# Performance work log

Hardware: AMD Instinct MI355X
Metric: run time of the kernel (lower is better)

## Reference

```python
import jax, jax.numpy as jnp
import numpy as np

B, D, Q, E, H, V = 32, 1024, 64, 384, 384, 50000
PAD = 0
EPS = 1e-12


def setup_inputs() -> dict:
    key = jax.random.key(0)
    ks = jax.random.split(key, 13)
    documents = jax.random.randint(ks[0], (B, D), 1, V)
    doc_lens = jax.random.randint(ks[1], (B,), D // 2, D + 1)
    doc_valid = jnp.arange(D)[None, :] < doc_lens[:, None]
    documents = jnp.where(doc_valid, documents, PAD)
    doc_masks = doc_valid.astype(jnp.float32)[:, :, None]
    querys = jax.random.randint(ks[2], (B, Q), 1, V)
    query_lens = jax.random.randint(ks[3], (B,), Q // 2, Q + 1)
    q_valid = jnp.arange(Q)[None, :] < query_lens[:, None]
    querys = jnp.where(q_valid, querys, PAD)
    query_masks = q_valid.astype(jnp.float32)[:, :, None]
    answers = documents[:, :1]  # guaranteed present in each doc
    emb = jax.random.uniform(ks[4], (V + 1, E), jnp.float32, -0.05, 0.05)
    emb = emb.at[PAD].set(0.0)
    gw = lambda k, s: jax.random.normal(k, s, jnp.float32) * 0.05
    w_ih_f = gw(ks[5], (3 * H, E)); w_hh_f = gw(ks[6], (3 * H, H))
    b_ih_f = gw(ks[7], (3 * H,)); b_hh_f = gw(ks[8], (3 * H,))
    w_ih_b = gw(ks[9], (3 * H, E)); w_hh_b = gw(ks[10], (3 * H, H))
    b_ih_b = gw(ks[11], (3 * H,)); b_hh_b = gw(ks[12], (3 * H,))
    return dict(documents=documents, doc_lens=doc_lens, doc_masks=doc_masks,
                querys=querys, query_lens=query_lens, query_masks=query_masks,
                answers=answers, emb=emb,
                w_ih_f=w_ih_f, w_hh_f=w_hh_f, b_ih_f=b_ih_f, b_hh_f=b_hh_f,
                w_ih_b=w_ih_b, w_hh_b=w_hh_b, b_ih_b=b_ih_b, b_hh_b=b_hh_b)


def _gru_dir(x, w_ih, w_hh, b_ih, b_hh):
    # x: [B,T,E] -> outputs [B,T,H]; torch GRU cell math
    Bn = x.shape[0]
    Hn = w_hh.shape[1]
    xp = jnp.einsum('bte,ge->btg', x, w_ih) + b_ih  # precompute input projections [B,T,3H]

    def step(h, g):
        gh = h @ w_hh.T + b_hh
        i_r, i_z, i_n = jnp.split(g, 3, axis=-1)
        h_r, h_z, h_n = jnp.split(gh, 3, axis=-1)
        r = jax.nn.sigmoid(i_r + h_r)
        z = jax.nn.sigmoid(i_z + h_z)
        n = jnp.tanh(i_n + r * h_n)
        hn = (1.0 - z) * n + z * h
        return hn, hn

    h0 = jnp.zeros((Bn, Hn), x.dtype)
    _, out = jax.lax.scan(step, h0, jnp.swapaxes(xp, 0, 1))
    return jnp.swapaxes(out, 0, 1)


def _rev_within_len(x, lens):
    # reverse each sequence only over its valid prefix (emulates packed bwd GRU)
    T = x.shape[1]
    t = jnp.arange(T)
    idx = jnp.where(t[None, :] < lens[:, None], lens[:, None] - 1 - t[None, :], t[None, :])
    return jnp.take_along_axis(x, idx[:, :, None], axis=1)


def _bigru(x, lens, valid, pf, pb):
    out_f = _gru_dir(x, *pf)
    out_b = _rev_within_len(_gru_dir(_rev_within_len(x, lens), *pb), lens)
    out = jnp.concatenate([out_f, out_b], axis=-1)
    return out * valid[:, :, None]  # unpack pads with zeros


def _softmax_mask(x, mask, axis):
    shift = jnp.max(x, axis=axis, keepdims=True)
    e = jnp.exp(x - shift) * mask
    return e / (jnp.sum(e, axis=axis, keepdims=True) + EPS)


def reference(documents, doc_lens, doc_masks, querys, query_lens, query_masks, answers,
              emb, w_ih_f, w_hh_f, b_ih_f, b_hh_f, w_ih_b, w_hh_b, b_ih_b, b_hh_b):
    doc_valid = doc_masks[..., 0]
    q_valid = query_masks[..., 0]
    doc_h = _bigru(emb[documents], doc_lens, doc_valid,
                   (w_ih_f, w_hh_f, b_ih_f, b_hh_f), (w_ih_b, w_hh_b, b_ih_b, b_hh_b))
    q_h = _bigru(emb[querys], query_lens, q_valid,
                 (w_ih_f, w_hh_f, b_ih_f, b_hh_f), (w_ih_b, w_hh_b, b_ih_b, b_hh_b))
    scores = jnp.einsum('bdh,bqh->bdq', doc_h, q_h)          # IndiATT_output
    pair_mask = jnp.einsum('bdo,bqo->bdq', doc_masks, query_masks)
    alpha = _softmax_mask(scores, pair_mask, axis=1)
    beta = _softmax_mask(scores, pair_mask, axis=2)
    beta_aver = jnp.sum(beta, axis=1) / doc_lens[:, None].astype(scores.dtype)  # [B,Q]
    s = jnp.einsum('bdq,bq->bd', alpha, beta_aver)            # AoA_output squeezed
    probs = jnp.sum(s * (documents == answers).astype(s.dtype), axis=1)

    def pick(doc, sv, vv):
        sc = jnp.zeros(V + 1, s.dtype).at[doc].add(sv * vv)   # segment-sum by word id
        cnt = jnp.zeros(V + 1, s.dtype).at[doc].add(vv)
        return jnp.argmax(jnp.where(cnt > 0, sc, -jnp.inf))

    pred_answers = jax.vmap(pick)(documents, s, doc_valid)
    return probs, pred_answers
```

## Files before the change

### kernel.cpp

```cpp
#include <hip/hip_runtime.h>
#include <hip/hip_bf16.h>
#include <stdint.h>

#define EPSV 1e-12f
#define NB 32
#define DD 1024
#define QQ 64
#define EE 384
#define HH 384
#define NW 12

typedef __attribute__((ext_vector_type(4))) float f32x4;
typedef __attribute__((ext_vector_type(8))) __bf16 bf16x8;
typedef __attribute__((ext_vector_type(4))) unsigned short u16x4;
typedef __attribute__((ext_vector_type(4))) int i32x4;
typedef unsigned short u16;

static __device__ __forceinline__ u16 f2bf(float f) {
  union { float f; uint32_t u; } v; v.f = f;
  uint32_t u = v.u;
  return (u16)((u + 0x7fffu + ((u >> 16) & 1u)) >> 16);
}

static __device__ __forceinline__ f32x4 MFMA(bf16x8 a, bf16x8 b, f32x4 c) {
  return __builtin_amdgcn_mfma_f32_16x16x32_bf16(a, b, c, 0, 0, 0);
}

static __device__ __forceinline__ void st_short_sc(u16* p, u16 v) {
  asm volatile("global_store_short %0, %1, off sc1" :: "v"(p), "v"((uint32_t)v) : "memory");
}
static __device__ __forceinline__ void ld_b128_sc(const u16* p, i32x4& d) {
  asm volatile("global_load_dwordx4 %0, %1, off sc1" : "=v"(d) : "v"(p) : "memory");
}

__global__ __launch_bounds__(256) void k_emb(const int* __restrict__ doc, const int* __restrict__ qry,
                                             const float* __restrict__ emb, u16* __restrict__ embx) {
  int i = blockIdx.x * 256 + threadIdx.x;
  int row = i / 96, e4 = i - row * 96;
  int tok = (row < NB * DD) ? doc[row] : qry[row - NB * DD];
  float4 v = ((const float4*)(emb + (size_t)tok * EE))[e4];
  u16x4 o; o.x = f2bf(v.x); o.y = f2bf(v.y); o.z = f2bf(v.z); o.w = f2bf(v.w);
  *(u16x4*)(embx + (size_t)row * EE + e4 * 4) = o;
}

__global__ __launch_bounds__(256) void k_rec(
    const u16* __restrict__ embx,
    const int* __restrict__ doc_lens, const int* __restrict__ q_lens,
    const float* __restrict__ w_ih_f, const float* __restrict__ w_hh_f,
    const float* __restrict__ b_ih_f, const float* __restrict__ b_hh_f,
    const float* __restrict__ w_ih_b, const float* __restrict__ w_hh_b,
    const float* __restrict__ b_ih_b, const float* __restrict__ b_hh_b,
    u16* __restrict__ doc_h, u16* __restrict__ q_h,
    u16* __restrict__ h_bc, unsigned* __restrict__ cnts) {
  __shared__ u16 wfrag[73728];
  __shared__ int lensh[32];

  const int grp = blockIdx.x / NW;
  const int wg = blockIdx.x - grp * NW;
  const int corpus = grp >> 1, dir = grp & 1;
  const int T = corpus ? QQ : DD;
  const int* lens = corpus ? q_lens : doc_lens;
  const float* w_ih = dir ? w_ih_b : w_ih_f;
  const float* w_hh = dir ? w_hh_b : w_hh_f;
  const float* b_ih = dir ? b_ih_b : b_ih_f;
  const float* b_hh = dir ? b_hh_b : b_hh_f;
  u16* out = corpus ? q_h : doc_h;
  const u16* ex_base = embx + (corpus ? (size_t)NB * DD * EE : 0);
  u16* hb = h_bc + (size_t)grp * (2 * NB * HH);
  unsigned* cnt = cnts + (size_t)grp * (1056 * 16);
  const int tid = threadIdx.x;

  if (tid < 32) lensh[tid] = lens[tid];
  for (int idx = tid; idx < 73728; idx += 256) {
    int nt = idx / 12288;
    int rem = idx - nt * 12288;
    int ks = rem >> 9;
    int le = rem & 511;
    int lane_ = le >> 3, i = le & 7;
    int g = nt >> 1, js_ = nt & 1;
    int colw = lane_ & 15, khiw = lane_ >> 4;
    int k = ks * 32 + khiw * 8 + i;
    int rowg = g * 384 + wg * 32 + js_ * 16 + colw;
    float v = (k < 384) ? w_ih[rowg * 384 + k] : w_hh[rowg * 384 + (k - 384)];
    wfrag[idx] = f2bf(v);
  }
  for (int idx = tid; idx < 1024; idx += 256) {
    int b = idx >> 5, jl_ = idx & 31;
    st_short_sc(hb + b * HH + wg * 32 + jl_, (u16)0);
  }
  asm volatile("s_waitcnt vmcnt(0)" ::: "memory");
  __syncthreads();
  if (tid == 0) {
    __hip_atomic_fetch_add(cnt, 1u, __ATOMIC_RELAXED, __HIP_MEMORY_SCOPE_AGENT);
    while (__hip_atomic_load(cnt, __ATOMIC_RELAXED, __HIP_MEMORY_SCOPE_AGENT) < (unsigned)NW)
      __builtin_amdgcn_s_sleep(1);
  }
  __syncthreads();

  const int lane = tid & 63, wv = tid >> 6;
  const int mt = wv >> 1, js = wv & 1;
  const int col = lane & 15, khi = lane >> 4;
  const int jg = wg * 32 + js * 16 + col;
  const float bias_r = b_ih[jg] + b_hh[jg];
  const float bias_z = b_ih[384 + jg] + b_hh[384 + jg];
  const float bias_in = b_ih[768 + jg];
  const float bias_hn = b_hh[768 + jg];
  const int b_x = mt * 16 + col;
  const int len_x = lensh[b_x];
  const int bh0 = mt * 16 + khi * 4;
  int len_h[4];
#pragma unroll
  for (int r = 0; r < 4; ++r) len_h[r] = lensh[bh0 + r];
  const u16* exrow = ex_base + (size_t)b_x * T * EE + khi * 8;
  u16* outp = out + (size_t)dir * HH + jg;
  f32x4 hprev{0.f, 0.f, 0.f, 0.f};

  auto trow_of = [&](int s) -> int { return dir ? ((s < len_x) ? (len_x - 1 - s) : s) : s; };
  auto load_ax = [&](bf16x8* ax, int s) {
    const u16* axp = exrow + (size_t)trow_of(s) * EE;
#pragma unroll
    for (int ks = 0; ks < 12; ++ks) ax[ks] = *(const bf16x8*)(axp + ks * 32);
  };

  bf16x8 axA[12], axB[12];
  load_ax(axA, 0);

  auto step = [&](int s, bf16x8* axc, bf16x8* axn) {
    const int p = s & 1;
    const u16* rbuf = hb + p * (NB * HH);
    u16* wbuf = hb + (p ^ 1) * (NB * HH);
    if (s + 1 < T) load_ax(axn, s + 1);
    i32x4 areg[12];
    const u16* ahp = rbuf + b_x * HH + khi * 8;
#pragma unroll
    for (int ks = 0; ks < 12; ++ks) ld_b128_sc(ahp + ks * 32, areg[ks]);
    f32x4 acc_r{0.f, 0.f, 0.f, 0.f};
    f32x4 acc_z = acc_r, acc_nx = acc_r, acc_nh = acc_r;
#pragma unroll
    for (int ks = 0; ks < 12; ++ks) {
      bf16x8 br = *(const bf16x8*)&wfrag[((js) * 24 + ks) * 512 + lane * 8];
      bf16x8 bz = *(const bf16x8*)&wfrag[((2 + js) * 24 + ks) * 512 + lane * 8];
      bf16x8 bn = *(const bf16x8*)&wfrag[((4 + js) * 24 + ks) * 512 + lane * 8];
      acc_r = MFMA(axc[ks], br, acc_r);
      acc_z = MFMA(axc[ks], bz, acc_z);
      acc_nx = MFMA(axc[ks], bn, acc_nx);
    }
    asm volatile("s_waitcnt vmcnt(0)" ::: "memory");
    __builtin_amdgcn_sched_barrier(0);
#pragma unroll
    for (int ks = 0; ks < 12; ++ks) {
      bf16x8 af = __builtin_bit_cast(bf16x8, areg[ks]);
      bf16x8 br = *(const bf16x8*)&wfrag[((js) * 24 + 12 + ks) * 512 + lane * 8];
      bf16x8 bz = *(const bf16x8*)&wfrag[((2 + js) * 24 + 12 + ks) * 512 + lane * 8];
      bf16x8 bn = *(const bf16x8*)&wfrag[((4 + js) * 24 + 12 + ks) * 512 + lane * 8];
      acc_r = MFMA(af, br, acc_r);
      acc_z = MFMA(af, bz, acc_z);
      acc_nh = MFMA(af, bn, acc_nh);
    }
#pragma unroll
    for (int r = 0; r < 4; ++r) {
      const int b = bh0 + r;
      float rg = 1.f / (1.f + __expf(-(acc_r[r] + bias_r)));
      float zg = 1.f / (1.f + __expf(-(acc_z[r] + bias_z)));
      float ng = tanhf(acc_nx[r] + bias_in + rg * (acc_nh[r] + bias_hn));
      float hn = (1.f - zg) * ng + zg * hprev[r];
      hprev[r] = hn;
      u16 hq = f2bf(hn);
      st_short_sc(wbuf + b * HH + jg, hq);
      const int len = len_h[r];
      const int tro = dir ? ((s < len) ? (len - 1 - s) : s) : s;
      outp[((size_t)b * T + tro) * (2 * HH)] = hq;
    }
    asm volatile("s_waitcnt vmcnt(0)" ::: "memory");
    __syncthreads();
    if (tid == 0) {
      unsigned* c = cnt + (size_t)(s + 1) * 16;
      __hip_atomic_fetch_add(c, 1u, __ATOMIC_RELAXED, __HIP_MEMORY_SCOPE_AGENT);
      while (__hip_atomic_load(c, __ATOMIC_RELAXED, __HIP_MEMORY_SCOPE_AGENT) < (unsigned)NW)
        __builtin_amdgcn_s_sleep(1);
    }
    __syncthreads();
  };

  for (int s = 0; s < T; s += 2) {
    step(s, axA, axB);
    step(s + 1, axB, axA);
  }
}

__global__ __launch_bounds__(256) void k_scores(
    const u16* __restrict__ doc_h, const u16* __restrict__ q_h,
    const int* __restrict__ doc_lens, const int* __restrict__ q_lens,
    float* __restrict__ SM, float* __restrict__ rowmax, float* __restrict__ rowsum) {
  const int b = blockIdx.x >> 4, dblk = blockIdx.x & 15;
  const int tid = threadIdx.x, lane = tid & 63, wv = tid >> 6;
  const int col = lane & 15, khi = lane >> 4;
  const int dlen = doc_lens[b], qlen = q_lens[b];
  const u16* dp = doc_h + ((size_t)(b * DD + dblk * 64 + wv * 16 + col)) * (2 * HH) + khi * 8;
  const u16* qp = q_h + (size_t)b * QQ * (2 * HH);
  f32x4 acc[4];
#pragma unroll
  for (int nt = 0; nt < 4; ++nt) acc[nt] = f32x4{0.f, 0.f, 0.f, 0.f};
  for (int ks = 0; ks < 24; ++ks) {
    bf16x8 av = *(const bf16x8*)(dp + ks * 32);
#pragma unroll
    for (int nt = 0; nt < 4; ++nt) {
      bf16x8 bv = *(const bf16x8*)(qp + (size_t)(nt * 16 + col) * (2 * HH) + ks * 32 + khi * 8);
      acc[nt] = MFMA(av, bv, acc[nt]);
    }
  }
  const int d0 = dblk * 64 + wv * 16 + khi * 4;
  float* smb = SM + (size_t)b * DD * QQ;
#pragma unroll
  for (int r = 0; r < 4; ++r) {
    const int d = d0 + r;
    const bool dv = d < dlen;
    float v[4];
#pragma unroll
    for (int nt = 0; nt < 4; ++nt) {
      const int q = nt * 16 + col;
      v[nt] = (dv && q < qlen) ? acc[nt][r] : 0.f;
      smb[(size_t)d * QQ + q] = v[nt];
    }
    float mx = fmaxf(fmaxf(v[0], v[1]), fmaxf(v[2], v[3]));
#pragma unroll
    for (int off = 1; off < 16; off <<= 1) mx = fmaxf(mx, __shfl_xor(mx, off, 64));
    float sm = 0.f;
#pragma unroll
    for (int nt = 0; nt < 4; ++nt) {
      const int q = nt * 16 + col;
      if (dv && q < qlen) sm += __expf(v[nt] - mx);
    }
#pragma unroll
    for (int off = 1; off < 16; off <<= 1) sm += __shfl_xor(sm, off, 64);
    if (col == 0) { rowmax[b * DD + d] = mx; rowsum[b * DD + d] = sm; }
  }
}

__global__ __launch_bounds__(256) void k_cols(
    const float* __restrict__ SM, const float* __restrict__ rowmax, const float* __restrict__ rowsum,
    const int* __restrict__ doc_lens, const int* __restrict__ q_lens,
    float* __restrict__ colmax, float* __restrict__ colsum, float* __restrict__ bav) {
  const int b = blockIdx.x, tid = threadIdx.x;
  const int q = tid & 63, dg = tid >> 6;
  __shared__ float red[4][64];
  __shared__ float cmx[64];
  const float* smb = SM + (size_t)b * DD * QQ;
  float cm = -3.0e38f;
  for (int d = dg; d < DD; d += 4) cm = fmaxf(cm, smb[(size_t)d * QQ + q]);
  red[dg][q] = cm;
  __syncthreads();
  if (tid < 64) cmx[tid] = fmaxf(fmaxf(red[0][tid], red[1][tid]), fmaxf(red[2][tid], red[3][tid]));
  __syncthreads();
  const int dlen = doc_lens[b];
  const bool qv = q < q_lens[b];
  const float cmq = cmx[q];
  float cs = 0.f, ba = 0.f;
  for (int d = dg; d < DD; d += 4) {
    if (qv && d < dlen) {
      float v = smb[(size_t)d * QQ + q];
      cs += __expf(v - cmq);
      ba += __expf(v - rowmax[b * DD + d]) / (rowsum[b * DD + d] + EPSV);
    }
  }
  __syncthreads();
  red[dg][q] = cs;
  __syncthreads();
  float cst = 0.f;
  if (tid < 64) cst = red[0][tid] + red[1][tid] + red[2][tid] + red[3][tid];
  __syncthreads();
  red[dg][q] = ba;
  __syncthreads();
  if (tid < 64) {
    float bat = red[0][tid] + red[1][tid] + red[2][tid] + red[3][tid];
    colmax[b * QQ + tid] = cmx[tid];
    colsum[b * QQ + tid] = cst;
    bav[b * QQ + tid] = bat / (float)dlen;
  }
}

__global__ __launch_bounds__(256) void k_s(
    const float* __restrict__ SM, const float* __restrict__ colmax, const float* __restrict__ colsum,
    const float* __restrict__ bav, const int* __restrict__ doc_lens, const int* __restrict__ q_lens,
    const int* __restrict__ documents, const int* __restrict__ answers,
    float* __restrict__ sc, float* __restrict__ cnt_tok, float* __restrict__ dout) {
  const int b = blockIdx.x >> 2, dblk = blockIdx.x & 3;
  const int tid = threadIdx.x;
  __shared__ float cm[64], cs[64], bv[64];
  __shared__ int qm[64];
  if (tid < 64) {
    cm[tid] = colmax[b * QQ + tid];
    cs[tid] = colsum[b * QQ + tid];
    bv[tid] = bav[b * QQ + tid];
    qm[tid] = (tid < q_lens[b]) ? 1 : 0;
  }
  __syncthreads();
  const int d = dblk * 256 + tid;
  const bool dv = d < doc_lens[b];
  const float* smr = SM + ((size_t)b * DD + d) * QQ;
  float sd = 0.f;
#pragma unroll
  for (int q = 0; q < 64; ++q) {
    float e = (dv && qm[q]) ? __expf(smr[q] - cm[q]) : 0.f;
    sd += e / (cs[q] + EPSV) * bv[q];
  }
  const int tok = documents[b * DD + d];
  if (tok == answers[b]) atomicAdd(&dout[b], sd);
  if (dv) {
    atomicAdd(&sc[(size_t)b * 50001 + tok], sd);
    atomicAdd(&cnt_tok[(size_t)b * 50001 + tok], 1.0f);
  }
}

__global__ __launch_bounds__(256) void k_pred(
    const float* __restrict__ sc, const float* __restrict__ cnt_tok, float* __restrict__ dout) {
  const int b = blockIdx.x, tid = threadIdx.x;
  __shared__ float bvs[256];
  __shared__ int bis[256];
  float bvv = -3.0e38f;
  int bii = 0x7fffffff;
  for (int i = tid; i < 50001; i += 256) {
    if (cnt_tok[(size_t)b * 50001 + i] > 0.f) {
      float v = sc[(size_t)b * 50001 + i];
      if (v > bvv) { bvv = v; bii = i; }
    }
  }
  bvs[tid] = bvv;
  bis[tid] = bii;
  __syncthreads();
  for (int st = 128; st > 0; st >>= 1) {
    if (tid < st) {
      float v2 = bvs[tid + st];
      int i2 = bis[tid + st];
      if (v2 > bvs[tid] || (v2 == bvs[tid] && i2 < bis[tid])) { bvs[tid] = v2; bis[tid] = i2; }
    }
    __syncthreads();
  }
  if (tid == 0) dout[32 + b] = (float)bis[0];
}

extern "C" void kernel_launch(void* const* d_in, const int* in_sizes, int n_in,
                              void* d_out, int out_size, void* d_ws, size_t ws_size,
                              hipStream_t stream) {
  const int* documents = (const int*)d_in[0];
  const int* doc_lens = (const int*)d_in[1];
  const int* querys = (const int*)d_in[3];
  const int* query_lens = (const int*)d_in[4];
  const int* answers = (const int*)d_in[6];
  const float* emb = (const float*)d_in[7];
  const float* w_ih_f = (const float*)d_in[8];
  const float* w_hh_f = (const float*)d_in[9];
  const float* b_ih_f = (const float*)d_in[10];
  const float* b_hh_f = (const float*)d_in[11];
  const float* w_ih_b = (const float*)d_in[12];
  const float* w_hh_b = (const float*)d_in[13];
  const float* b_ih_b = (const float*)d_in[14];
  const float* b_hh_b = (const float*)d_in[15];
  float* dout = (float*)d_out;
  char* ws = (char*)d_ws;

  size_t o = 0;
  auto alloc = [&](size_t bytes) { size_t r = o; o += (bytes + 255) & ~(size_t)255; return r; };
  size_t o_embx = alloc((size_t)34816 * 384 * 2);
  size_t o_doch = alloc((size_t)NB * DD * 768 * 2);
  size_t o_qh   = alloc((size_t)NB * QQ * 768 * 2);
  size_t o_hbc  = alloc((size_t)4 * 2 * NB * HH * 2);
  size_t o_cnt  = alloc((size_t)4 * 1056 * 16 * 4);
  size_t o_SM   = alloc((size_t)NB * DD * QQ * 4);
  size_t o_rmax = alloc((size_t)NB * DD * 4);
  size_t o_rsum = alloc((size_t)NB * DD * 4);
  size_t o_cmax = alloc((size_t)NB * QQ * 4);
  size_t o_csum = alloc((size_t)NB * QQ * 4);
  size_t o_bav  = alloc((size_t)NB * QQ * 4);
  size_t o_sc   = alloc((size_t)NB * 50001 * 4);
  size_t o_ctk  = alloc((size_t)NB * 50001 * 4);
  (void)ws_size; (void)in_sizes; (void)n_in; (void)out_size;

  hipMemsetAsync(ws + o_cnt, 0, (size_t)4 * 1056 * 16 * 4, stream);
  hipMemsetAsync(ws + o_sc, 0, (o_ctk - o_sc) + (size_t)NB * 50001 * 4, stream);
  hipMemsetAsync(d_out, 0, 64 * sizeof(float), stream);

  k_emb<<<13056, 256, 0, stream>>>(documents, querys, emb, (u16*)(ws + o_embx));
  k_rec<<<48, 256, 0, stream>>>((u16*)(ws + o_embx), doc_lens, query_lens,
                                w_ih_f, w_hh_f, b_ih_f, b_hh_f,
                                w_ih_b, w_hh_b, b_ih_b, b_hh_b,
                                (u16*)(ws + o_doch), (u16*)(ws + o_qh),
                                (u16*)(ws + o_hbc), (unsigned*)(ws + o_cnt));
  k_scores<<<512, 256, 0, stream>>>((u16*)(ws + o_doch), (u16*)(ws + o_qh), doc_lens, query_lens,
                                    (float*)(ws + o_SM), (float*)(ws + o_rmax), (float*)(ws + o_rsum));
  k_cols<<<32, 256, 0, stream>>>((float*)(ws + o_SM), (float*)(ws + o_rmax), (float*)(ws + o_rsum),
                                 doc_lens, query_lens,
                                 (float*)(ws + o_cmax), (float*)(ws + o_csum), (float*)(ws + o_bav));
  k_s<<<128, 256, 0, stream>>>((float*)(ws + o_SM), (float*)(ws + o_cmax), (float*)(ws + o_csum),
                               (float*)(ws + o_bav), doc_lens, query_lens, documents, answers,
                               (float*)(ws + o_sc), (float*)(ws + o_ctk), dout);
  k_pred<<<32, 256, 0, stream>>>((float*)(ws + o_sc), (float*)(ws + o_ctk), dout);
}
```

Before: 6.000 ms.

## Hoist GRU input projections into chunked parallel kernel, shrink recurrent grid

The input projection (x·W_ih) is moved out of the sequential GRU loop into a separate parallel MFMA kernel that writes fp32 gate pre-activations in chunks of 256 timesteps. The recurrent kernel now does only the h·W_hh product with 4 workgroups per direction instead of 12, so fewer blocks take part in each per-step global barrier. The r-gate weights stay in registers and the z and n gate weights sit in LDS. Hidden state is carried across four launches through a global buffer. This cuts per-step MFMA work and sync fan-in, but each workgroup handles more columns per step, and the change adds launches and xp memory traffic.

```diff
diff --git a/kernel.cpp b/kernel.cpp
--- a/kernel.cpp
+++ b/kernel.cpp
@@ -8,7 +8,8 @@
 #define QQ 64
 #define EE 384
 #define HH 384
-#define NW 12
+#define NWR 4
+#define CH 256
 
 typedef __attribute__((ext_vector_type(4))) float f32x4;
 typedef __attribute__((ext_vector_type(8))) __bf16 bf16x8;
@@ -24,6 +25,15 @@
 
 static __device__ __forceinline__ f32x4 MFMA(bf16x8 a, bf16x8 b, f32x4 c) {
   return __builtin_amdgcn_mfma_f32_16x16x32_bf16(a, b, c, 0, 0, 0);
+}
+
+static __device__ __forceinline__ bf16x8 ldw8(const float* p) {
+  float4 a = *(const float4*)p;
+  float4 b = *(const float4*)(p + 4);
+  union { u16 e[8]; bf16x8 v; } u;
+  u.e[0] = f2bf(a.x); u.e[1] = f2bf(a.y); u.e[2] = f2bf(a.z); u.e[3] = f2bf(a.w);
+  u.e[4] = f2bf(b.x); u.e[5] = f2bf(b.y); u.e[6] = f2bf(b.z); u.e[7] = f2bf(b.w);
+  return u.v;
 }
 
 static __device__ __forceinline__ void st_short_sc(u16* p, u16 v) {
@@ -43,149 +53,223 @@
   *(u16x4*)(embx + (size_t)row * EE + e4 * 4) = o;
 }
 
-__global__ __launch_bounds__(256) void k_rec(
-    const u16* __restrict__ embx,
+__global__ __launch_bounds__(512, 2) void k_xp(
+    const u16* __restrict__ embx, const int* __restrict__ doc_lens, const int* __restrict__ q_lens,
+    const float* __restrict__ w_ih_f, const float* __restrict__ b_ih_f, const float* __restrict__ b_hh_f,
+    const float* __restrict__ w_ih_b, const float* __restrict__ b_ih_b, const float* __restrict__ b_hh_b,
+    float* __restrict__ xpd, float* __restrict__ xpq, int cbase) {
+  __shared__ int lensh[32];
+  const int gx = blockIdx.x;
+  int corpus, d2, jblk, tch;
+  if (gx < 48) { corpus = 0; d2 = gx / 24; int rem = gx % 24; jblk = rem / 4; tch = rem % 4; }
+  else { corpus = 1; int g2 = gx - 48; d2 = g2 / 6; jblk = g2 % 6; tch = 0; }
+  const int T = corpus ? QQ : DD;
+  const int* lens = corpus ? q_lens : doc_lens;
+  const float* w_ih = d2 ? w_ih_b : w_ih_f;
+  const float* b_ih = d2 ? b_ih_b : b_ih_f;
+  const float* b_hh = d2 ? b_hh_b : b_hh_f;
+  const u16* exb = embx + (corpus ? (size_t)NB * DD * EE : 0);
+  float* xpg = corpus ? (xpq + (size_t)d2 * QQ * 36864) : (xpd + (size_t)d2 * CH * 36864);
+  const int tid = threadIdx.x;
+  if (tid < 32) lensh[tid] = lens[tid];
+  __syncthreads();
+  const int lane = tid & 63, wv = tid >> 6;
+  const int wslot = wv >> 1, mt = wv & 1;
+  const int col = lane & 15, khi = lane >> 4;
+  const int jg = jblk * 64 + wslot * 16 + col;
+  const float br = b_ih[jg] + b_hh[jg];
+  const float bz = b_ih[384 + jg] + b_hh[384 + jg];
+  const float bn = b_ih[768 + jg];
+  bf16x8 Wr[12], Wz[12], Wn[12];
+#pragma unroll
+  for (int ks = 0; ks < 12; ++ks) {
+    Wr[ks] = ldw8(w_ih + (size_t)jg * 384 + ks * 32 + khi * 8);
+    Wz[ks] = ldw8(w_ih + (size_t)(384 + jg) * 384 + ks * 32 + khi * 8);
+    Wn[ks] = ldw8(w_ih + (size_t)(768 + jg) * 384 + ks * 32 + khi * 8);
+  }
+  const int b_a = mt * 16 + col;
+  const int lenb = lensh[b_a];
+  const int bh0 = mt * 16 + khi * 4;
+  for (int tt = 0; tt < 64; ++tt) {
+    const int s_lc = tch * 64 + tt;
+    const int s_g = corpus ? s_lc : (cbase + s_lc);
+    const int trow = d2 ? ((s_g < lenb) ? (lenb - 1 - s_g) : s_g) : s_g;
+    const u16* ap = exb + ((size_t)b_a * T + trow) * EE + khi * 8;
+    bf16x8 A[12];
+#pragma unroll
+    for (int ks = 0; ks < 12; ++ks) A[ks] = *(const bf16x8*)(ap + ks * 32);
+    f32x4 ar{0.f, 0.f, 0.f, 0.f}, az = ar, an = ar;
+#pragma unroll
+    for (int ks = 0; ks < 12; ++ks) {
+      ar = MFMA(A[ks], Wr[ks], ar);
+      az = MFMA(A[ks], Wz[ks], az);
+      an = MFMA(A[ks], Wn[ks], an);
+    }
+    float* op = xpg + (size_t)s_lc * 36864 + (size_t)jg * 32 + bh0;
+    f32x4 o0{ar[0] + br, ar[1] + br, ar[2] + br, ar[3] + br};
+    f32x4 o1{az[0] + bz, az[1] + bz, az[2] + bz, az[3] + bz};
+    f32x4 o2{an[0] + bn, an[1] + bn, an[2] + bn, an[3] + bn};
+    *(f32x4*)op = o0;
+    *(f32x4*)(op + 384 * 32) = o1;
+    *(f32x4*)(op + 768 * 32) = o2;
+  }
+}
+
+__global__ __launch_bounds__(384, 2) void k_rec(
+    const float* __restrict__ xpd, const float* __restrict__ xpq,
     const int* __restrict__ doc_lens, const int* __restrict__ q_lens,
-    const float* __restrict__ w_ih_f, const float* __restrict__ w_hh_f,
-    const float* __restrict__ b_ih_f, const float* __restrict__ b_hh_f,
-    const float* __restrict__ w_ih_b, const float* __restrict__ w_hh_b,
-    const float* __restrict__ b_ih_b, const float* __restrict__ b_hh_b,
+    const float* __restrict__ w_hh_f, const float* __restrict__ b_hh_f,
+    const float* __restrict__ w_hh_b, const float* __restrict__ b_hh_b,
     u16* __restrict__ doc_h, u16* __restrict__ q_h,
-    u16* __restrict__ h_bc, unsigned* __restrict__ cnts) {
-  __shared__ u16 wfrag[73728];
+    u16* __restrict__ h_bc, unsigned* __restrict__ cnts,
+    float* __restrict__ h_state, int cbase, int first) {
+  __shared__ u16 wz_lds[36864];
+  __shared__ u16 wn_lds[36864];
   __shared__ int lensh[32];
-
-  const int grp = blockIdx.x / NW;
-  const int wg = blockIdx.x - grp * NW;
+  const int grp = blockIdx.x >> 2, wg = blockIdx.x & 3;
   const int corpus = grp >> 1, dir = grp & 1;
   const int T = corpus ? QQ : DD;
+  const int nst = corpus ? QQ : CH;
   const int* lens = corpus ? q_lens : doc_lens;
-  const float* w_ih = dir ? w_ih_b : w_ih_f;
   const float* w_hh = dir ? w_hh_b : w_hh_f;
-  const float* b_ih = dir ? b_ih_b : b_ih_f;
   const float* b_hh = dir ? b_hh_b : b_hh_f;
   u16* out = corpus ? q_h : doc_h;
-  const u16* ex_base = embx + (corpus ? (size_t)NB * DD * EE : 0);
+  const float* xpg = corpus ? (xpq + (size_t)dir * QQ * 36864) : (xpd + (size_t)dir * CH * 36864);
   u16* hb = h_bc + (size_t)grp * (2 * NB * HH);
   unsigned* cnt = cnts + (size_t)grp * (1056 * 16);
   const int tid = threadIdx.x;
-
   if (tid < 32) lensh[tid] = lens[tid];
-  for (int idx = tid; idx < 73728; idx += 256) {
-    int nt = idx / 12288;
-    int rem = idx - nt * 12288;
+  for (int idx = tid; idx < 36864; idx += 384) {
+    int w_ = idx / 6144;
+    int rem = idx - w_ * 6144;
     int ks = rem >> 9;
     int le = rem & 511;
     int lane_ = le >> 3, i = le & 7;
-    int g = nt >> 1, js_ = nt & 1;
-    int colw = lane_ & 15, khiw = lane_ >> 4;
-    int k = ks * 32 + khiw * 8 + i;
-    int rowg = g * 384 + wg * 32 + js_ * 16 + colw;
-    float v = (k < 384) ? w_ih[rowg * 384 + k] : w_hh[rowg * 384 + (k - 384)];
-    wfrag[idx] = f2bf(v);
-  }
-  for (int idx = tid; idx < 1024; idx += 256) {
-    int b = idx >> 5, jl_ = idx & 31;
-    st_short_sc(hb + b * HH + wg * 32 + jl_, (u16)0);
-  }
-  asm volatile("s_waitcnt vmcnt(0)" ::: "memory");
-  __syncthreads();
-  if (tid == 0) {
-    __hip_atomic_fetch_add(cnt, 1u, __ATOMIC_RELAXED, __HIP_MEMORY_SCOPE_AGENT);
-    while (__hip_atomic_load(cnt, __ATOMIC_RELAXED, __HIP_MEMORY_SCOPE_AGENT) < (unsigned)NW)
-      __builtin_amdgcn_s_sleep(1);
-  }
-  __syncthreads();
-
-  const int lane = tid & 63, wv = tid >> 6;
-  const int mt = wv >> 1, js = wv & 1;
+    int dim = wg * 96 + w_ * 16 + (lane_ & 15);
+    int k = ks * 32 + (lane_ >> 4) * 8 + i;
+    wz_lds[idx] = f2bf(w_hh[(size_t)(384 + dim) * 384 + k]);
+    wn_lds[idx] = f2bf(w_hh[(size_t)(768 + dim) * 384 + k]);
+  }
+  const int lane = tid & 63, w = tid >> 6;
   const int col = lane & 15, khi = lane >> 4;
-  const int jg = wg * 32 + js * 16 + col;
-  const float bias_r = b_ih[jg] + b_hh[jg];
-  const float bias_z = b_ih[384 + jg] + b_hh[384 + jg];
-  const float bias_in = b_ih[768 + jg];
-  const float bias_hn = b_hh[768 + jg];
-  const int b_x = mt * 16 + col;
-  const int len_x = lensh[b_x];
-  const int bh0 = mt * 16 + khi * 4;
-  int len_h[4];
-#pragma unroll
-  for (int r = 0; r < 4; ++r) len_h[r] = lensh[bh0 + r];
-  const u16* exrow = ex_base + (size_t)b_x * T * EE + khi * 8;
-  u16* outp = out + (size_t)dir * HH + jg;
-  f32x4 hprev{0.f, 0.f, 0.f, 0.f};
-
-  auto trow_of = [&](int s) -> int { return dir ? ((s < len_x) ? (len_x - 1 - s) : s) : s; };
-  auto load_ax = [&](bf16x8* ax, int s) {
-    const u16* axp = exrow + (size_t)trow_of(s) * EE;
-#pragma unroll
-    for (int ks = 0; ks < 12; ++ks) ax[ks] = *(const bf16x8*)(axp + ks * 32);
-  };
-
-  bf16x8 axA[12], axB[12];
-  load_ax(axA, 0);
-
-  auto step = [&](int s, bf16x8* axc, bf16x8* axn) {
+  const int dimr = wg * 96 + w * 16 + col;
+  const float bhhn = b_hh[768 + dimr];
+  bf16x8 Wr[12];
+#pragma unroll
+  for (int ks = 0; ks < 12; ++ks) Wr[ks] = ldw8(w_hh + (size_t)dimr * 384 + ks * 32 + khi * 8);
+  if (first) {
+#pragma unroll
+    for (int mt = 0; mt < 2; ++mt)
+#pragma unroll
+      for (int r = 0; r < 4; ++r) st_short_sc(hb + (mt * 16 + khi * 4 + r) * HH + dimr, (u16)0);
+    asm volatile("s_waitcnt vmcnt(0)" ::: "memory");
+  }
+  __syncthreads();
+  int len8[2][4];
+  float hprev[2][4];
+#pragma unroll
+  for (int mt = 0; mt < 2; ++mt)
+#pragma unroll
+    for (int r = 0; r < 4; ++r) {
+      const int b = mt * 16 + khi * 4 + r;
+      len8[mt][r] = lensh[b];
+      hprev[mt][r] = first ? 0.f : h_state[(size_t)grp * 12288 + (size_t)dimr * 32 + b];
+    }
+  if (first) {
+    if (tid == 0) {
+      __hip_atomic_fetch_add(cnt, 1u, __ATOMIC_RELAXED, __HIP_MEMORY_SCOPE_AGENT);
+      while (__hip_atomic_load(cnt, __ATOMIC_RELAXED, __HIP_MEMORY_SCOPE_AGENT) < (unsigned)NWR)
+        __builtin_amdgcn_s_sleep(1);
+    }
+    __syncthreads();
+  }
+  u16* outp = out + (size_t)dir * HH + dimr;
+  f32x4 xp[2][3];
+  {
+    const float* xs = xpg + (size_t)dimr * 32;
+#pragma unroll
+    for (int mt = 0; mt < 2; ++mt)
+#pragma unroll
+      for (int g = 0; g < 3; ++g)
+        xp[mt][g] = *(const f32x4*)(xs + (size_t)g * 384 * 32 + mt * 16 + khi * 4);
+  }
+
+  for (int s = cbase; s < cbase + nst; ++s) {
     const int p = s & 1;
-    const u16* rbuf = hb + p * (NB * HH);
-    u16* wbuf = hb + (p ^ 1) * (NB * HH);
-    if (s + 1 < T) load_ax(axn, s + 1);
-    i32x4 areg[12];
-    const u16* ahp = rbuf + b_x * HH + khi * 8;
-#pragma unroll
-    for (int ks = 0; ks < 12; ++ks) ld_b128_sc(ahp + ks * 32, areg[ks]);
-    f32x4 acc_r{0.f, 0.f, 0.f, 0.f};
-    f32x4 acc_z = acc_r, acc_nx = acc_r, acc_nh = acc_r;
-#pragma unroll
-    for (int ks = 0; ks < 12; ++ks) {
-      bf16x8 br = *(const bf16x8*)&wfrag[((js) * 24 + ks) * 512 + lane * 8];
-      bf16x8 bz = *(const bf16x8*)&wfrag[((2 + js) * 24 + ks) * 512 + lane * 8];
-      bf16x8 bn = *(const bf16x8*)&wfrag[((4 + js) * 24 + ks) * 512 + lane * 8];
-      acc_r = MFMA(axc[ks], br, acc_r);
-      acc_z = MFMA(axc[ks], bz, acc_z);
-      acc_nx = MFMA(axc[ks], bn, acc_nx);
+    const u16* rb = hb + p * (NB * HH);
+    u16* wb = hb + (p ^ 1) * (NB * HH);
+    i32x4 areg[2][12];
+#pragma unroll
+    for (int mt = 0; mt < 2; ++mt) {
+      const u16* ap = rb + (mt * 16 + col) * HH + khi * 8;
+#pragma unroll
+      for (int ks = 0; ks < 12; ++ks) ld_b128_sc(ap + ks * 32, areg[mt][ks]);
     }
     asm volatile("s_waitcnt vmcnt(0)" ::: "memory");
     __builtin_amdgcn_sched_barrier(0);
-#pragma unroll
-    for (int ks = 0; ks < 12; ++ks) {
-      bf16x8 af = __builtin_bit_cast(bf16x8, areg[ks]);
-      bf16x8 br = *(const bf16x8*)&wfrag[((js) * 24 + 12 + ks) * 512 + lane * 8];
-      bf16x8 bz = *(const bf16x8*)&wfrag[((2 + js) * 24 + 12 + ks) * 512 + lane * 8];
-      bf16x8 bn = *(const bf16x8*)&wfrag[((4 + js) * 24 + 12 + ks) * 512 + lane * 8];
-      acc_r = MFMA(af, br, acc_r);
-      acc_z = MFMA(af, bz, acc_z);
-      acc_nh = MFMA(af, bn, acc_nh);
-    }
-#pragma unroll
-    for (int r = 0; r < 4; ++r) {
-      const int b = bh0 + r;
-      float rg = 1.f / (1.f + __expf(-(acc_r[r] + bias_r)));
-      float zg = 1.f / (1.f + __expf(-(acc_z[r] + bias_z)));
-      float ng = tanhf(acc_nx[r] + bias_in + rg * (acc_nh[r] + bias_hn));
-      float hn = (1.f - zg) * ng + zg * hprev[r];
-      hprev[r] = hn;
-      u16 hq = f2bf(hn);
-      st_short_sc(wbuf + b * HH + jg, hq);
-      const int len = len_h[r];
-      const int tro = dir ? ((s < len) ? (len - 1 - s) : s) : s;
-      outp[((size_t)b * T + tro) * (2 * HH)] = hq;
-    }
-    asm volatile("s_waitcnt vmcnt(0)" ::: "memory");
-    __syncthreads();
+    f32x4 accr[2], accz[2], accn[2];
+#pragma unroll
+    for (int mt = 0; mt < 2; ++mt) { accr[mt] = f32x4{0.f,0.f,0.f,0.f}; accz[mt] = accr[mt]; accn[mt] = accr[mt]; }
+#pragma unroll
+    for (int mt = 0; mt < 2; ++mt)
+#pragma unroll
+      for (int ks = 0; ks < 12; ++ks) {
+        bf16x8 af = __builtin_bit_cast(bf16x8, areg[mt][ks]);
+        accr[mt] = MFMA(af, Wr[ks], accr[mt]);
+        bf16x8 bz = *(const bf16x8*)&wz_lds[((w * 12 + ks) * 64 + lane) * 8];
+        accz[mt] = MFMA(af, bz, accz[mt]);
+        bf16x8 bn = *(const bf16x8*)&wn_lds[((w * 12 + ks) * 64 + lane) * 8];
+        accn[mt] = MFMA(af, bn, accn[mt]);
+      }
+    u16 hq[2][4];
+#pragma unroll
+    for (int mt = 0; mt < 2; ++mt)
+#pragma unroll
+      for (int r = 0; r < 4; ++r) {
+        const int b = mt * 16 + khi * 4 + r;
+        float rg = 1.f / (1.f + __expf(-(accr[mt][r] + xp[mt][0][r])));
+        float zg = 1.f / (1.f + __expf(-(accz[mt][r] + xp[mt][1][r])));
+        float ng = tanhf(xp[mt][2][r] + rg * (accn[mt][r] + bhhn));
+        float hn = (1.f - zg) * ng + zg * hprev[mt][r];
+        hprev[mt][r] = hn;
+        hq[mt][r] = f2bf(hn);
+        st_short_sc(wb + b * HH + dimr, hq[mt][r]);
+      }
+    {
+      const int sp = (s + 1 < cbase + nst) ? (s + 1 - cbase) : (nst - 1);
+      const float* xs = xpg + (size_t)sp * 36864 + (size_t)dimr * 32;
+#pragma unroll
+      for (int mt = 0; mt < 2; ++mt)
+#pragma unroll
+        for (int g = 0; g < 3; ++g)
+          xp[mt][g] = *(const f32x4*)(xs + (size_t)g * 384 * 32 + mt * 16 + khi * 4);
+    }
+#pragma unroll
+    for (int mt = 0; mt < 2; ++mt)
+#pragma unroll
+      for (int r = 0; r < 4; ++r) {
+        const int b = mt * 16 + khi * 4 + r;
+        const int len = len8[mt][r];
+        const int tro = dir ? ((s < len) ? (len - 1 - s) : s) : s;
+        outp[((size_t)b * T + tro) * (2 * HH)] = hq[mt][r];
+      }
+    asm volatile("s_waitcnt vmcnt(14)" ::: "memory");
+    __builtin_amdgcn_s_barrier();
     if (tid == 0) {
       unsigned* c = cnt + (size_t)(s + 1) * 16;
       __hip_atomic_fetch_add(c, 1u, __ATOMIC_RELAXED, __HIP_MEMORY_SCOPE_AGENT);
-      while (__hip_atomic_load(c, __ATOMIC_RELAXED, __HIP_MEMORY_SCOPE_AGENT) < (unsigned)NW)
+      while (__hip_atomic_load(c, __ATOMIC_RELAXED, __HIP_MEMORY_SCOPE_AGENT) < (unsigned)NWR)
         __builtin_amdgcn_s_sleep(1);
     }
-    __syncthreads();
-  };
-
-  for (int s = 0; s < T; s += 2) {
-    step(s, axA, axB);
-    step(s + 1, axB, axA);
-  }
+    __builtin_amdgcn_s_barrier();
+  }
+#pragma unroll
+  for (int mt = 0; mt < 2; ++mt)
+#pragma unroll
+    for (int r = 0; r < 4; ++r) {
+      const int b = mt * 16 + khi * 4 + r;
+      h_state[(size_t)grp * 12288 + (size_t)dimr * 32 + b] = hprev[mt][r];
+    }
 }
 
 __global__ __launch_bounds__(256) void k_scores(
@@ -362,9 +446,12 @@
   size_t o = 0;
   auto alloc = [&](size_t bytes) { size_t r = o; o += (bytes + 255) & ~(size_t)255; return r; };
   size_t o_embx = alloc((size_t)34816 * 384 * 2);
+  size_t o_xpd  = alloc((size_t)2 * CH * 36864 * 4);
+  size_t o_xpq  = alloc((size_t)2 * QQ * 36864 * 4);
   size_t o_doch = alloc((size_t)NB * DD * 768 * 2);
   size_t o_qh   = alloc((size_t)NB * QQ * 768 * 2);
   size_t o_hbc  = alloc((size_t)4 * 2 * NB * HH * 2);
+  size_t o_hst  = alloc((size_t)4 * HH * NB * 4);
   size_t o_cnt  = alloc((size_t)4 * 1056 * 16 * 4);
   size_t o_SM   = alloc((size_t)NB * DD * QQ * 4);
   size_t o_rmax = alloc((size_t)NB * DD * 4);
@@ -381,11 +468,19 @@
   hipMemsetAsync(d_out, 0, 64 * sizeof(float), stream);
 
   k_emb<<<13056, 256, 0, stream>>>(documents, querys, emb, (u16*)(ws + o_embx));
-  k_rec<<<48, 256, 0, stream>>>((u16*)(ws + o_embx), doc_lens, query_lens,
-                                w_ih_f, w_hh_f, b_ih_f, b_hh_f,
-                                w_ih_b, w_hh_b, b_ih_b, b_hh_b,
-                                (u16*)(ws + o_doch), (u16*)(ws + o_qh),
-                                (u16*)(ws + o_hbc), (unsigned*)(ws + o_cnt));
+  for (int c = 0; c < 4; ++c) {
+    const int cbase = c * CH;
+    k_xp<<<c == 0 ? 60 : 48, 512, 0, stream>>>(
+        (u16*)(ws + o_embx), doc_lens, query_lens,
+        w_ih_f, b_ih_f, b_hh_f, w_ih_b, b_ih_b, b_hh_b,
+        (float*)(ws + o_xpd), (float*)(ws + o_xpq), cbase);
+    k_rec<<<c == 0 ? 16 : 8, 384, 0, stream>>>(
+        (float*)(ws + o_xpd), (float*)(ws + o_xpq), doc_lens, query_lens,
+        w_hh_f, b_hh_f, w_hh_b, b_hh_b,
+        (u16*)(ws + o_doch), (u16*)(ws + o_qh),
+        (u16*)(ws + o_hbc), (unsigned*)(ws + o_cnt),
+        (float*)(ws + o_hst), cbase, c == 0 ? 1 : 0);
+  }
   k_scores<<<512, 256, 0, stream>>>((u16*)(ws + o_doch), (u16*)(ws + o_qh), doc_lens, query_lens,
                                     (float*)(ws + o_SM), (float*)(ws + o_rmax), (float*)(ws + o_rsum));
   k_cols<<<32, 256, 0, stream>>>((float*)(ws + o_SM), (float*)(ws + o_rmax), (float*)(ws + o_rsum),
```

Result: slower. 13.28 ms (+121.4%).

## Replace per-step workgroup barrier and atomic counter with per-wave tag flags

Applied to the files above, without the earlier changes.

The GRU recurrence kernel no longer ends each step with __syncthreads, a global atomic increment and a single-thread spin. Instead each wave publishes a monotonically increasing step tag after its hidden-state stores. Before loading the previous hidden state, each wave polls only the tags of the waves that produce its batch rows. The input-projection MFMAs now run before the poll, and the next-step embedding load is issued after the hidden-state load, so independent work overlaps the wait. This relies on careful memory ordering through sc1 loads and stores, and it adds polling traffic from every wave.

```diff
diff --git a/kernel.cpp b/kernel.cpp
--- a/kernel.cpp
+++ b/kernel.cpp
@@ -31,6 +31,22 @@
 }
 static __device__ __forceinline__ void ld_b128_sc(const u16* p, i32x4& d) {
   asm volatile("global_load_dwordx4 %0, %1, off sc1" : "=v"(d) : "v"(p) : "memory");
+}
+static __device__ __forceinline__ void st_dword_sc(unsigned* p, unsigned v) {
+  asm volatile("global_store_dword %0, %1, off sc1" :: "v"(p), "v"(v) : "memory");
+}
+static __device__ __forceinline__ void ld_tags(const unsigned* p, i32x4& a, i32x4& b, i32x4& c,
+                                               i32x4& d, i32x4& e, i32x4& f) {
+  asm volatile(
+      "global_load_dwordx4 %0, %6, off sc1\n\t"
+      "global_load_dwordx4 %1, %6, off offset:16 sc1\n\t"
+      "global_load_dwordx4 %2, %6, off offset:32 sc1\n\t"
+      "global_load_dwordx4 %3, %6, off offset:48 sc1\n\t"
+      "global_load_dwordx4 %4, %6, off offset:64 sc1\n\t"
+      "global_load_dwordx4 %5, %6, off offset:80 sc1\n\t"
+      "s_waitcnt vmcnt(0)"
+      : "=&v"(a), "=&v"(b), "=&v"(c), "=&v"(d), "=&v"(e), "=&v"(f)
+      : "v"(p) : "memory");
 }
 
 __global__ __launch_bounds__(256) void k_emb(const int* __restrict__ doc, const int* __restrict__ qry,
@@ -51,7 +67,7 @@
     const float* __restrict__ w_ih_b, const float* __restrict__ w_hh_b,
     const float* __restrict__ b_ih_b, const float* __restrict__ b_hh_b,
     u16* __restrict__ doc_h, u16* __restrict__ q_h,
-    u16* __restrict__ h_bc, unsigned* __restrict__ cnts) {
+    u16* __restrict__ h_bc, unsigned* __restrict__ cnts, unsigned* __restrict__ tags) {
   __shared__ u16 wfrag[73728];
   __shared__ int lensh[32];
 
@@ -67,7 +83,7 @@
   u16* out = corpus ? q_h : doc_h;
   const u16* ex_base = embx + (corpus ? (size_t)NB * DD * EE : 0);
   u16* hb = h_bc + (size_t)grp * (2 * NB * HH);
-  unsigned* cnt = cnts + (size_t)grp * (1056 * 16);
+  unsigned* cnt = cnts + (size_t)grp * 16;
   const int tid = threadIdx.x;
 
   if (tid < 32) lensh[tid] = lens[tid];
@@ -115,11 +131,30 @@
   u16* outp = out + (size_t)dir * HH + jg;
   f32x4 hprev{0.f, 0.f, 0.f, 0.f};
 
+  const unsigned* tagrow = tags + (size_t)grp * 64 + mt * 32;
+  unsigned* tagp = tags + (size_t)grp * 64 + mt * 32 + (wg * 2 + js);
+
   auto trow_of = [&](int s) -> int { return dir ? ((s < len_x) ? (len_x - 1 - s) : s) : s; };
   auto load_ax = [&](bf16x8* ax, int s) {
     const u16* axp = exrow + (size_t)trow_of(s) * EE;
 #pragma unroll
     for (int ks = 0; ks < 12; ++ks) ax[ks] = *(const bf16x8*)(axp + ks * 32);
+  };
+  auto umin2 = [](unsigned a, unsigned b) { return a < b ? a : b; };
+  auto pollwait = [&](unsigned need) {
+    while (true) {
+      i32x4 t0, t1, t2, t3, t4, t5;
+      ld_tags(tagrow, t0, t1, t2, t3, t4, t5);
+      unsigned mn = 0xffffffffu;
+#pragma unroll
+      for (int k = 0; k < 4; ++k) {
+        mn = umin2(mn, (unsigned)t0[k]); mn = umin2(mn, (unsigned)t1[k]);
+        mn = umin2(mn, (unsigned)t2[k]); mn = umin2(mn, (unsigned)t3[k]);
+        mn = umin2(mn, (unsigned)t4[k]); mn = umin2(mn, (unsigned)t5[k]);
+      }
+      if (mn >= need) break;
+      __builtin_amdgcn_s_sleep(1);
+    }
   };
 
   bf16x8 axA[12], axB[12];
@@ -129,11 +164,6 @@
     const int p = s & 1;
     const u16* rbuf = hb + p * (NB * HH);
     u16* wbuf = hb + (p ^ 1) * (NB * HH);
-    if (s + 1 < T) load_ax(axn, s + 1);
-    i32x4 areg[12];
-    const u16* ahp = rbuf + b_x * HH + khi * 8;
-#pragma unroll
-    for (int ks = 0; ks < 12; ++ks) ld_b128_sc(ahp + ks * 32, areg[ks]);
     f32x4 acc_r{0.f, 0.f, 0.f, 0.f};
     f32x4 acc_z = acc_r, acc_nx = acc_r, acc_nh = acc_r;
 #pragma unroll
@@ -145,8 +175,14 @@
       acc_z = MFMA(axc[ks], bz, acc_z);
       acc_nx = MFMA(axc[ks], bn, acc_nx);
     }
+    pollwait((unsigned)s);
+    i32x4 areg[12];
+    const u16* ahp = rbuf + b_x * HH + khi * 8;
+#pragma unroll
+    for (int ks = 0; ks < 12; ++ks) ld_b128_sc(ahp + ks * 32, areg[ks]);
     asm volatile("s_waitcnt vmcnt(0)" ::: "memory");
     __builtin_amdgcn_sched_barrier(0);
+    if (s + 1 < T) load_ax(axn, s + 1);
 #pragma unroll
     for (int ks = 0; ks < 12; ++ks) {
       bf16x8 af = __builtin_bit_cast(bf16x8, areg[ks]);
@@ -157,6 +193,7 @@
       acc_z = MFMA(af, bz, acc_z);
       acc_nh = MFMA(af, bn, acc_nh);
     }
+    u16 hq[4];
 #pragma unroll
     for (int r = 0; r < 4; ++r) {
       const int b = bh0 + r;
@@ -165,21 +202,18 @@
       float ng = tanhf(acc_nx[r] + bias_in + rg * (acc_nh[r] + bias_hn));
       float hn = (1.f - zg) * ng + zg * hprev[r];
       hprev[r] = hn;
-      u16 hq = f2bf(hn);
-      st_short_sc(wbuf + b * HH + jg, hq);
+      hq[r] = f2bf(hn);
+      st_short_sc(wbuf + b * HH + jg, hq[r]);
+    }
+    asm volatile("s_waitcnt vmcnt(0)" ::: "memory");
+    if (lane == 0) st_dword_sc(tagp, (unsigned)(s + 1));
+#pragma unroll
+    for (int r = 0; r < 4; ++r) {
+      const int b = bh0 + r;
       const int len = len_h[r];
       const int tro = dir ? ((s < len) ? (len - 1 - s) : s) : s;
-      outp[((size_t)b * T + tro) * (2 * HH)] = hq;
-    }
-    asm volatile("s_waitcnt vmcnt(0)" ::: "memory");
-    __syncthreads();
-    if (tid == 0) {
-      unsigned* c = cnt + (size_t)(s + 1) * 16;
-      __hip_atomic_fetch_add(c, 1u, __ATOMIC_RELAXED, __HIP_MEMORY_SCOPE_AGENT);
-      while (__hip_atomic_load(c, __ATOMIC_RELAXED, __HIP_MEMORY_SCOPE_AGENT) < (unsigned)NW)
-        __builtin_amdgcn_s_sleep(1);
-    }
-    __syncthreads();
+      outp[((size_t)b * T + tro) * (2 * HH)] = hq[r];
+    }
   };
 
   for (int s = 0; s < T; s += 2) {
@@ -365,7 +399,9 @@
   size_t o_doch = alloc((size_t)NB * DD * 768 * 2);
   size_t o_qh   = alloc((size_t)NB * QQ * 768 * 2);
   size_t o_hbc  = alloc((size_t)4 * 2 * NB * HH * 2);
-  size_t o_cnt  = alloc((size_t)4 * 1056 * 16 * 4);
+  size_t o_cnt  = alloc((size_t)4 * 16 * 4);
+  size_t o_tag  = alloc((size_t)4 * 64 * 4);
+  size_t o_sync_end = o;
   size_t o_SM   = alloc((size_t)NB * DD * QQ * 4);
   size_t o_rmax = alloc((size_t)NB * DD * 4);
   size_t o_rsum = alloc((size_t)NB * DD * 4);
@@ -376,7 +412,7 @@
   size_t o_ctk  = alloc((size_t)NB * 50001 * 4);
   (void)ws_size; (void)in_sizes; (void)n_in; (void)out_size;
 
-  hipMemsetAsync(ws + o_cnt, 0, (size_t)4 * 1056 * 16 * 4, stream);
+  hipMemsetAsync(ws + o_cnt, 0, o_sync_end - o_cnt, stream);
   hipMemsetAsync(ws + o_sc, 0, (o_ctk - o_sc) + (size_t)NB * 50001 * 4, stream);
   hipMemsetAsync(d_out, 0, 64 * sizeof(float), stream);
 
@@ -385,7 +421,7 @@
                                 w_ih_f, w_hh_f, b_ih_f, b_hh_f,
                                 w_ih_b, w_hh_b, b_ih_b, b_hh_b,
                                 (u16*)(ws + o_doch), (u16*)(ws + o_qh),
-                                (u16*)(ws + o_hbc), (unsigned*)(ws + o_cnt));
+                                (u16*)(ws + o_hbc), (unsigned*)(ws + o_cnt), (unsigned*)(ws + o_tag));
   k_scores<<<512, 256, 0, stream>>>((u16*)(ws + o_doch), (u16*)(ws + o_qh), doc_lens, query_lens,
                                     (float*)(ws + o_SM), (float*)(ws + o_rmax), (float*)(ws + o_rsum));
   k_cols<<<32, 256, 0, stream>>>((float*)(ws + o_SM), (float*)(ws + o_rmax), (float*)(ws + o_rsum),
```

Measured after the change: 5.691 ms. -5.2%, faster.

## Replace per-step grid barrier with sentinel-flagged hidden-state history polling

Applied to the files above, without the earlier changes.

The recurrent kernel no longer uses an atomic counter barrier after each timestep. Each timestep's hidden state is written to its own slice of a full-history buffer that starts filled with 0xFFFF. Consumers poll that slice until no sentinel values remain, so each workgroup waits only on the data it needs instead of a global barrier. This costs a large extra memset of the history buffer and spin-reloads of global memory. It also treats the bf16 pattern 0xFFFF (a NaN) as 'not ready', so a genuine NaN in the hidden state would make consumers spin forever. The next-step input embedding load is moved after the wait.

```diff
diff --git a/kernel.cpp b/kernel.cpp
--- a/kernel.cpp
+++ b/kernel.cpp
@@ -29,8 +29,26 @@
 static __device__ __forceinline__ void st_short_sc(u16* p, u16 v) {
   asm volatile("global_store_short %0, %1, off sc1" :: "v"(p), "v"((uint32_t)v) : "memory");
 }
-static __device__ __forceinline__ void ld_b128_sc(const u16* p, i32x4& d) {
-  asm volatile("global_load_dwordx4 %0, %1, off sc1" : "=v"(d) : "v"(p) : "memory");
+static __device__ __forceinline__ void ld_h12(const u16* p,
+    i32x4& d0, i32x4& d1, i32x4& d2, i32x4& d3, i32x4& d4, i32x4& d5,
+    i32x4& d6, i32x4& d7, i32x4& d8, i32x4& d9, i32x4& d10, i32x4& d11) {
+  asm volatile(
+      "global_load_dwordx4 %0, %12, off sc1\n\t"
+      "global_load_dwordx4 %1, %12, off offset:64 sc1\n\t"
+      "global_load_dwordx4 %2, %12, off offset:128 sc1\n\t"
+      "global_load_dwordx4 %3, %12, off offset:192 sc1\n\t"
+      "global_load_dwordx4 %4, %12, off offset:256 sc1\n\t"
+      "global_load_dwordx4 %5, %12, off offset:320 sc1\n\t"
+      "global_load_dwordx4 %6, %12, off offset:384 sc1\n\t"
+      "global_load_dwordx4 %7, %12, off offset:448 sc1\n\t"
+      "global_load_dwordx4 %8, %12, off offset:512 sc1\n\t"
+      "global_load_dwordx4 %9, %12, off offset:576 sc1\n\t"
+      "global_load_dwordx4 %10, %12, off offset:640 sc1\n\t"
+      "global_load_dwordx4 %11, %12, off offset:704 sc1\n\t"
+      "s_waitcnt vmcnt(0)"
+      : "=&v"(d0), "=&v"(d1), "=&v"(d2), "=&v"(d3), "=&v"(d4), "=&v"(d5),
+        "=&v"(d6), "=&v"(d7), "=&v"(d8), "=&v"(d9), "=&v"(d10), "=&v"(d11)
+      : "v"(p) : "memory");
 }
 
 __global__ __launch_bounds__(256) void k_emb(const int* __restrict__ doc, const int* __restrict__ qry,
@@ -51,7 +69,7 @@
     const float* __restrict__ w_ih_b, const float* __restrict__ w_hh_b,
     const float* __restrict__ b_ih_b, const float* __restrict__ b_hh_b,
     u16* __restrict__ doc_h, u16* __restrict__ q_h,
-    u16* __restrict__ h_bc, unsigned* __restrict__ cnts) {
+    u16* __restrict__ h_all, unsigned* __restrict__ cnts) {
   __shared__ u16 wfrag[73728];
   __shared__ int lensh[32];
 
@@ -66,8 +84,8 @@
   const float* b_hh = dir ? b_hh_b : b_hh_f;
   u16* out = corpus ? q_h : doc_h;
   const u16* ex_base = embx + (corpus ? (size_t)NB * DD * EE : 0);
-  u16* hb = h_bc + (size_t)grp * (2 * NB * HH);
-  unsigned* cnt = cnts + (size_t)grp * (1056 * 16);
+  u16* ha = h_all + (size_t)grp * ((DD + 1) * NB * HH);
+  unsigned* cnt = cnts + (size_t)grp * 16;
   const int tid = threadIdx.x;
 
   if (tid < 32) lensh[tid] = lens[tid];
@@ -86,7 +104,7 @@
   }
   for (int idx = tid; idx < 1024; idx += 256) {
     int b = idx >> 5, jl_ = idx & 31;
-    st_short_sc(hb + b * HH + wg * 32 + jl_, (u16)0);
+    st_short_sc(ha + (size_t)b * HH + wg * 32 + jl_, (u16)0);
   }
   asm volatile("s_waitcnt vmcnt(0)" ::: "memory");
   __syncthreads();
@@ -126,14 +144,6 @@
   load_ax(axA, 0);
 
   auto step = [&](int s, bf16x8* axc, bf16x8* axn) {
-    const int p = s & 1;
-    const u16* rbuf = hb + p * (NB * HH);
-    u16* wbuf = hb + (p ^ 1) * (NB * HH);
-    if (s + 1 < T) load_ax(axn, s + 1);
-    i32x4 areg[12];
-    const u16* ahp = rbuf + b_x * HH + khi * 8;
-#pragma unroll
-    for (int ks = 0; ks < 12; ++ks) ld_b128_sc(ahp + ks * 32, areg[ks]);
     f32x4 acc_r{0.f, 0.f, 0.f, 0.f};
     f32x4 acc_z = acc_r, acc_nx = acc_r, acc_nh = acc_r;
 #pragma unroll
@@ -145,8 +155,27 @@
       acc_z = MFMA(axc[ks], bz, acc_z);
       acc_nx = MFMA(axc[ks], bn, acc_nx);
     }
-    asm volatile("s_waitcnt vmcnt(0)" ::: "memory");
+    const u16* ahp = ha + (size_t)s * (NB * HH) + (size_t)b_x * HH + khi * 8;
+    i32x4 a0, a1, a2, a3, a4, a5, a6, a7, a8, a9, a10, a11;
+    while (true) {
+      ld_h12(ahp, a0, a1, a2, a3, a4, a5, a6, a7, a8, a9, a10, a11);
+      uint32_t bad = 0;
+      auto chk = [&](const i32x4& d) {
+#pragma unroll
+        for (int k = 0; k < 4; ++k) {
+          uint32_t u = (uint32_t)d[k];
+          bad |= ((u & 0xFFFFu) == 0xFFFFu);
+          bad |= ((u >> 16) == 0xFFFFu);
+        }
+      };
+      chk(a0); chk(a1); chk(a2); chk(a3); chk(a4); chk(a5);
+      chk(a6); chk(a7); chk(a8); chk(a9); chk(a10); chk(a11);
+      if (__all(bad == 0)) break;
+      __builtin_amdgcn_s_sleep(1);
+    }
     __builtin_amdgcn_sched_barrier(0);
+    if (s + 1 < T) load_ax(axn, s + 1);
+    i32x4 areg[12] = {a0, a1, a2, a3, a4, a5, a6, a7, a8, a9, a10, a11};
 #pragma unroll
     for (int ks = 0; ks < 12; ++ks) {
       bf16x8 af = __builtin_bit_cast(bf16x8, areg[ks]);
@@ -157,6 +186,8 @@
       acc_z = MFMA(af, bz, acc_z);
       acc_nh = MFMA(af, bn, acc_nh);
     }
+    u16 hq[4];
+    u16* wslice = ha + (size_t)(s + 1) * (NB * HH);
 #pragma unroll
     for (int r = 0; r < 4; ++r) {
       const int b = bh0 + r;
@@ -165,21 +196,16 @@
       float ng = tanhf(acc_nx[r] + bias_in + rg * (acc_nh[r] + bias_hn));
       float hn = (1.f - zg) * ng + zg * hprev[r];
       hprev[r] = hn;
-      u16 hq = f2bf(hn);
-      st_short_sc(wbuf + b * HH + jg, hq);
+      hq[r] = f2bf(hn);
+      st_short_sc(wslice + (size_t)b * HH + jg, hq[r]);
+    }
+#pragma unroll
+    for (int r = 0; r < 4; ++r) {
+      const int b = bh0 + r;
       const int len = len_h[r];
       const int tro = dir ? ((s < len) ? (len - 1 - s) : s) : s;
-      outp[((size_t)b * T + tro) * (2 * HH)] = hq;
-    }
-    asm volatile("s_waitcnt vmcnt(0)" ::: "memory");
-    __syncthreads();
-    if (tid == 0) {
-      unsigned* c = cnt + (size_t)(s + 1) * 16;
-      __hip_atomic_fetch_add(c, 1u, __ATOMIC_RELAXED, __HIP_MEMORY_SCOPE_AGENT);
-      while (__hip_atomic_load(c, __ATOMIC_RELAXED, __HIP_MEMORY_SCOPE_AGENT) < (unsigned)NW)
-        __builtin_amdgcn_s_sleep(1);
-    }
-    __syncthreads();
+      outp[((size_t)b * T + tro) * (2 * HH)] = hq[r];
+    }
   };
 
   for (int s = 0; s < T; s += 2) {
@@ -362,10 +388,10 @@
   size_t o = 0;
   auto alloc = [&](size_t bytes) { size_t r = o; o += (bytes + 255) & ~(size_t)255; return r; };
   size_t o_embx = alloc((size_t)34816 * 384 * 2);
+  size_t o_hall = alloc((size_t)4 * (DD + 1) * NB * HH * 2);
   size_t o_doch = alloc((size_t)NB * DD * 768 * 2);
   size_t o_qh   = alloc((size_t)NB * QQ * 768 * 2);
-  size_t o_hbc  = alloc((size_t)4 * 2 * NB * HH * 2);
-  size_t o_cnt  = alloc((size_t)4 * 1056 * 16 * 4);
+  size_t o_cnt  = alloc((size_t)4 * 16 * 4);
   size_t o_SM   = alloc((size_t)NB * DD * QQ * 4);
   size_t o_rmax = alloc((size_t)NB * DD * 4);
   size_t o_rsum = alloc((size_t)NB * DD * 4);
@@ -376,7 +402,8 @@
   size_t o_ctk  = alloc((size_t)NB * 50001 * 4);
   (void)ws_size; (void)in_sizes; (void)n_in; (void)out_size;
 
-  hipMemsetAsync(ws + o_cnt, 0, (size_t)4 * 1056 * 16 * 4, stream);
+  hipMemsetAsync(ws + o_hall, 0xFF, (size_t)4 * (DD + 1) * NB * HH * 2, stream);
+  hipMemsetAsync(ws + o_cnt, 0, (size_t)4 * 16 * 4, stream);
   hipMemsetAsync(ws + o_sc, 0, (o_ctk - o_sc) + (size_t)NB * 50001 * 4, stream);
   hipMemsetAsync(d_out, 0, 64 * sizeof(float), stream);
 
@@ -385,7 +412,7 @@
                                 w_ih_f, w_hh_f, b_ih_f, b_hh_f,
                                 w_ih_b, w_hh_b, b_ih_b, b_hh_b,
                                 (u16*)(ws + o_doch), (u16*)(ws + o_qh),
-                                (u16*)(ws + o_hbc), (unsigned*)(ws + o_cnt));
+                                (u16*)(ws + o_hall), (unsigned*)(ws + o_cnt));
   k_scores<<<512, 256, 0, stream>>>((u16*)(ws + o_doch), (u16*)(ws + o_qh), doc_lens, query_lens,
                                     (float*)(ws + o_SM), (float*)(ws + o_rmax), (float*)(ws + o_rsum));
   k_cols<<<32, 256, 0, stream>>>((float*)(ws + o_SM), (float*)(ws + o_rmax), (float*)(ws + o_rsum),
```

Measured after the change: 5.670 ms. 1.06x faster.
